# Performance work log

Hardware: AMD Instinct MI355X
Metric: run time of the kernel (lower is better)

The kernel has to match this reference:

```python
import jax, jax.numpy as jnp
import numpy as np

H, N, F = 10, 200000, 128
HID, C = 256, 100
NEG_SLOPE = 0.2

def _leaky(x):
    return jnp.where(x >= 0, x, NEG_SLOPE * x)

def _prelu(x, a):
    return jnp.where(x >= 0, x, a * x)

def setup_inputs() -> dict:
    key = jax.random.key(0)
    ks = jax.random.split(key, 12)
    inp = {
        "features": jax.random.normal(ks[0], (H, N, F), dtype=jnp.float32),
        "label_emb": jax.random.normal(ks[1], (N, C), dtype=jnp.float32),
        # lr_att: Linear(2F, 1) -> weight as [2F] vector + scalar bias
        "W_att": jax.random.normal(ks[2], (2 * F,), dtype=jnp.float32) * 0.05,
        "b_att": jnp.zeros((), dtype=jnp.float32),
        # lr_output = FeedForwardNetII(F, HID, C, n_layers=2): Dense(F,HID), PReLU, Dense(HID,C)
        "Wo1": jax.random.normal(ks[3], (F, HID), dtype=jnp.float32) * 0.05,
        "bo1": jnp.zeros((HID,), dtype=jnp.float32),
        "ao": jnp.asarray(0.25, dtype=jnp.float32),
        "Wo2": jax.random.normal(ks[4], (HID, C), dtype=jnp.float32) * 0.05,
        "bo2": jnp.zeros((C,), dtype=jnp.float32),
        # label_fc = FeedForwardNet(C, HID, C, n_layers=2): Linear(C,HID), PReLU, Linear(HID,C)
        "Wl1": jax.random.normal(ks[5], (C, HID), dtype=jnp.float32) * 0.05,
        "bl1": jnp.zeros((HID,), dtype=jnp.float32),
        "al": jnp.asarray(0.25, dtype=jnp.float32),
        "Wl2": jax.random.normal(ks[6], (HID, C), dtype=jnp.float32) * 0.05,
        "bl2": jnp.zeros((C,), dtype=jnp.float32),
    }
    return inp

def reference(features, label_emb, W_att, b_att, Wo1, bo1, ao, Wo2, bo2,
              Wl1, bl1, al, Wl2, bl2):
    # features: [H, N, F]; dropouts are identity (p=0, eval mode)
    nF = features.shape[-1]
    W1, W2 = W_att[:nF], W_att[nF:]  # cat([history, x_i]) @ W_att == history@W1 + x_i@W2
    x0 = features[0]
    scores = [_leaky(x0 @ (W1 + W2) + b_att)]  # hop 0: cat([x0, x0])
    for i in range(1, features.shape[0]):
        hist_att = jax.nn.softmax(jnp.stack(scores, axis=1), axis=1)  # [N, i]
        history = jnp.einsum('ni,inf->nf', hist_att, features[:i])    # [N, F]
        scores.append(_leaky(history @ W1 + features[i] @ W2 + b_att))
    att = jax.nn.softmax(jnp.stack(scores, axis=1), axis=1)           # [N, H]
    right = jnp.einsum('ni,inf->nf', att, features)                   # [N, F]
    # lr_output: Dense -> PReLU -> Dense
    out = _prelu(right @ Wo1 + bo1, ao) @ Wo2 + bo2                   # [N, C]
    # label branch: label_fc(label_emb)
    out = out + (_prelu(label_emb @ Wl1 + bl1, al) @ Wl2 + bl2)
    return out
```

## Files before the change

kernel.cpp:

```cpp
#include <hip/hip_runtime.h>
#include <cstddef>

#define NHOP 10
#define NN 200000
#define FF 128
#define HIDD 256
#define CCC 100
#define NEG_SLOPE_C 0.2f

typedef __attribute__((ext_vector_type(8))) short bf16x8;
typedef __attribute__((ext_vector_type(4))) short bf16x4;
typedef __attribute__((ext_vector_type(4))) float f32x4;

__device__ __forceinline__ unsigned short f2bf(float x){
  unsigned u = __float_as_uint(x);
  u = u + 0x7FFFu + ((u >> 16) & 1u);
  return (unsigned short)(u >> 16);
}
__device__ __forceinline__ float bf2f(short s){
  return __uint_as_float(((unsigned)(unsigned short)s) << 16);
}

__device__ __forceinline__ f32x4 mfma16(bf16x8 a, bf16x8 b, f32x4 c){
  return __builtin_amdgcn_mfma_f32_16x16x32_bf16(a, b, c, 0, 0, 0);
}

__device__ __forceinline__ float leakyf(float x){ return x >= 0.f ? x : NEG_SLOPE_C*x; }

__global__ __launch_bounds__(256) void prep_weights(
    const float* __restrict__ Wo1, const float* __restrict__ Wl1,
    const float* __restrict__ Wo2, const float* __restrict__ Wl2,
    unsigned short* __restrict__ Wo1T, unsigned short* __restrict__ Wl1T,
    unsigned short* __restrict__ Wo2T, unsigned short* __restrict__ Wl2T)
{
  const int id = blockIdx.x*256 + threadIdx.x;
  {
    const int c = id >> 7, k = id & 127;
    Wo1T[id] = f2bf(Wo1[(size_t)k*HIDD + c]);
    Wl1T[id] = (k < CCC) ? f2bf(Wl1[(size_t)k*HIDD + c]) : 0;
  }
  if (id < 112*256){
    const int c = id >> 8, k = id & 255;
    Wo2T[id] = (c < CCC) ? f2bf(Wo2[(size_t)k*CCC + c]) : 0;
    Wl2T[id] = (c < CCC) ? f2bf(Wl2[(size_t)k*CCC + c]) : 0;
  }
}

__global__ __launch_bounds__(256) void attn_right_kernel(
    const float* __restrict__ feat,
    const float* __restrict__ Watt,
    const float* __restrict__ batt,
    unsigned short* __restrict__ rightb)
{
  const int lane = threadIdx.x & 63;
  const int w = threadIdx.x >> 6;
  const int nl = lane >> 4, fl = lane & 15;
  const int n = blockIdx.x*16 + w*4 + nl;

  const float4 w1a = *reinterpret_cast<const float4*>(Watt + fl*4);
  const float4 w1b = *reinterpret_cast<const float4*>(Watt + 64 + fl*4);
  const float4 w2a = *reinterpret_cast<const float4*>(Watt + FF + fl*4);
  const float4 w2b = *reinterpret_cast<const float4*>(Watt + FF + 64 + fl*4);
  const float b = batt[0];

  float p1[NHOP], p2[NHOP];
  bf16x8 fbf[NHOP];
  const float* fp = feat + (size_t)n*FF;
  #pragma unroll
  for (int i=0;i<NHOP;i++){
    const float* hp = fp + (size_t)i*((size_t)NN*FF);
    const float4 va = *reinterpret_cast<const float4*>(hp + fl*4);
    const float4 vb = *reinterpret_cast<const float4*>(hp + 64 + fl*4);
    p1[i] = va.x*w1a.x + va.y*w1a.y + va.z*w1a.z + va.w*w1a.w
          + vb.x*w1b.x + vb.y*w1b.y + vb.z*w1b.z + vb.w*w1b.w;
    p2[i] = va.x*w2a.x + va.y*w2a.y + va.z*w2a.z + va.w*w2a.w
          + vb.x*w2b.x + vb.y*w2b.y + vb.z*w2b.z + vb.w*w2b.w;
    fbf[i][0]=(short)f2bf(va.x); fbf[i][1]=(short)f2bf(va.y);
    fbf[i][2]=(short)f2bf(va.z); fbf[i][3]=(short)f2bf(va.w);
    fbf[i][4]=(short)f2bf(vb.x); fbf[i][5]=(short)f2bf(vb.y);
    fbf[i][6]=(short)f2bf(vb.z); fbf[i][7]=(short)f2bf(vb.w);
  }
  #pragma unroll
  for (int m=8;m>0;m>>=1){
    #pragma unroll
    for (int i=0;i<NHOP;i++){
      p1[i] += __shfl_xor(p1[i], m, 64);
      p2[i] += __shfl_xor(p2[i], m, 64);
    }
  }
  float sc[NHOP];
  sc[0] = leakyf(p1[0] + p2[0] + b);
  #pragma unroll
  for (int i=1;i<NHOP;i++){
    float mx = sc[0];
    #pragma unroll
    for (int j=1;j<i;j++) mx = fmaxf(mx, sc[j]);
    float Z = 0.f, hs = 0.f;
    #pragma unroll
    for (int j=0;j<i;j++){
      const float e = __expf(sc[j]-mx);
      Z += e;
      hs = fmaf(e, p1[j], hs);
    }
    sc[i] = leakyf(hs/Z + p2[i] + b);
  }
  float mx = sc[0];
  #pragma unroll
  for (int j=1;j<NHOP;j++) mx = fmaxf(mx, sc[j]);
  float Z = 0.f;
  float e[NHOP];
  #pragma unroll
  for (int j=0;j<NHOP;j++){ e[j] = __expf(sc[j]-mx); Z += e[j]; }
  const float inv = 1.f/Z;
  float racc[8];
  #pragma unroll
  for (int u=0;u<8;u++) racc[u] = 0.f;
  #pragma unroll
  for (int j=0;j<NHOP;j++){
    const float a = e[j]*inv;
    #pragma unroll
    for (int u=0;u<8;u++) racc[u] = fmaf(a, bf2f(fbf[j][u]), racc[u]);
  }
  bf16x4 sa, sb;
  sa[0]=(short)f2bf(racc[0]); sa[1]=(short)f2bf(racc[1]);
  sa[2]=(short)f2bf(racc[2]); sa[3]=(short)f2bf(racc[3]);
  sb[0]=(short)f2bf(racc[4]); sb[1]=(short)f2bf(racc[5]);
  sb[2]=(short)f2bf(racc[6]); sb[3]=(short)f2bf(racc[7]);
  *reinterpret_cast<bf16x4*>(rightb + (size_t)n*FF + fl*4) = sa;
  *reinterpret_cast<bf16x4*>(rightb + (size_t)n*FF + 64 + fl*4) = sb;
}

__device__ __forceinline__ void scatter_h(unsigned short* sH, f32x4 h, float bias,
                                          float alpha, int c, int nt, int lq)
{
  #pragma unroll
  for (int j=0;j<4;++j){
    float v = h[j] + bias;
    v = v >= 0.f ? v : alpha*v;
    const int n = nt*16 + lq*4 + j;
    *reinterpret_cast<unsigned short*>((char*)sH + n*512 + ((2*c) ^ ((n&7)<<4))) = f2bf(v);
  }
}

__device__ __forceinline__ void gemm2_accum(const unsigned short* sH,
    const unsigned short* __restrict__ W2T, f32x4 (&o)[2][4],
    const int w, const int lr, const int lq)
{
  #pragma unroll
  for (int i2=0; i2<2; ++i2){
    const int ct2 = 2*w + i2;
    if (ct2 < 7){
      bf16x8 b2[8];
      #pragma unroll
      for (int kk=0; kk<8; ++kk)
        b2[kk] = *reinterpret_cast<const bf16x8*>(W2T + (size_t)(ct2*16+lr)*256 + kk*32 + lq*8);
      #pragma unroll
      for (int nt=0; nt<4; ++nt){
        const int row = nt*16 + lr;
        #pragma unroll
        for (int kk=0; kk<8; ++kk){
          const bf16x8 a2 = *reinterpret_cast<const bf16x8*>(
              (const char*)sH + row*512 + ((kk*64 + lq*16) ^ ((row&7)<<4)));
          o[i2][nt] = mfma16(a2, b2[kk], o[i2][nt]);
        }
      }
    }
  }
}

__device__ __forceinline__ bf16x8 label_frag(const float* __restrict__ label,
                                             size_t gnode, int kk, int lq)
{
  bf16x8 r = (bf16x8){0,0,0,0,0,0,0,0};
  const float* base = label + gnode*CCC;
  if (kk < 3){
    const float4 va = *reinterpret_cast<const float4*>(base + kk*32 + lq*8);
    const float4 vb = *reinterpret_cast<const float4*>(base + kk*32 + lq*8 + 4);
    r[0]=(short)f2bf(va.x); r[1]=(short)f2bf(va.y); r[2]=(short)f2bf(va.z); r[3]=(short)f2bf(va.w);
    r[4]=(short)f2bf(vb.x); r[5]=(short)f2bf(vb.y); r[6]=(short)f2bf(vb.z); r[7]=(short)f2bf(vb.w);
  } else if (lq == 0){
    const float4 va = *reinterpret_cast<const float4*>(base + 96);
    r[0]=(short)f2bf(va.x); r[1]=(short)f2bf(va.y); r[2]=(short)f2bf(va.z); r[3]=(short)f2bf(va.w);
  }
  return r;
}

__global__ __launch_bounds__(256) void mlp_mfma_kernel(
    const unsigned short* __restrict__ rightb, const float* __restrict__ label,
    const unsigned short* __restrict__ Wo1T, const float* __restrict__ bo1, const float* __restrict__ aop,
    const unsigned short* __restrict__ Wo2T, const float* __restrict__ bo2,
    const unsigned short* __restrict__ Wl1T, const float* __restrict__ bl1, const float* __restrict__ alp,
    const unsigned short* __restrict__ Wl2T, const float* __restrict__ bl2,
    float* __restrict__ out)
{
  __shared__ __align__(16) unsigned short sH[64*256];
  const int t = threadIdx.x;
  const int w = t >> 6, lane = t & 63, lr = lane & 15, lq = lane >> 4;
  const size_t nb = (size_t)blockIdx.x * 64;
  const float ao = aop[0], al = alp[0];

  f32x4 o[2][4];
  #pragma unroll
  for (int i2=0; i2<2; ++i2){
    const int ct2 = 2*w + i2;
    const int c2 = ct2*16 + lr;
    const float init = (ct2 < 7 && c2 < CCC) ? (bo2[c2] + bl2[c2]) : 0.f;
    #pragma unroll
    for (int nt=0; nt<4; ++nt) o[i2][nt] = (f32x4){init, init, init, init};
  }

  #pragma unroll
  for (int cc=0; cc<2; ++cc){
    bf16x8 B[2][4];
    float b1c[2];
    #pragma unroll
    for (int ct=0; ct<2; ++ct){
      const int c = (w*4 + cc*2 + ct)*16 + lr;
      b1c[ct] = bo1[c];
      #pragma unroll
      for (int kk=0; kk<4; ++kk)
        B[ct][kk] = *reinterpret_cast<const bf16x8*>(Wo1T + (size_t)c*128 + kk*32 + lq*8);
    }
    #pragma unroll
    for (int nt=0; nt<4; ++nt){
      const int row = nt*16 + lr;
      f32x4 h0 = (f32x4){0.f,0.f,0.f,0.f}, h1 = h0;
      #pragma unroll
      for (int kk=0; kk<4; ++kk){
        const bf16x8 a = *reinterpret_cast<const bf16x8*>(
            rightb + (nb + row)*FF + kk*32 + lq*8);
        h0 = mfma16(a, B[0][kk], h0);
        h1 = mfma16(a, B[1][kk], h1);
      }
      scatter_h(sH, h0, b1c[0], ao, (w*4 + cc*2 + 0)*16 + lr, nt, lq);
      scatter_h(sH, h1, b1c[1], ao, (w*4 + cc*2 + 1)*16 + lr, nt, lq);
    }
  }
  __syncthreads();
  gemm2_accum(sH, Wo2T, o, w, lr, lq);
  __syncthreads();

  #pragma unroll
  for (int cc=0; cc<2; ++cc){
    bf16x8 B[2][4];
    float b1c[2];
    #pragma unroll
    for (int ct=0; ct<2; ++ct){
      const int c = (w*4 + cc*2 + ct)*16 + lr;
      b1c[ct] = bl1[c];
      #pragma unroll
      for (int kk=0; kk<4; ++kk)
        B[ct][kk] = *reinterpret_cast<const bf16x8*>(Wl1T + (size_t)c*128 + kk*32 + lq*8);
    }
    #pragma unroll
    for (int nt=0; nt<4; ++nt){
      const int row = nt*16 + lr;
      f32x4 h0 = (f32x4){0.f,0.f,0.f,0.f}, h1 = h0;
      #pragma unroll
      for (int kk=0; kk<4; ++kk){
        const bf16x8 a = label_frag(label, nb + row, kk, lq);
        h0 = mfma16(a, B[0][kk], h0);
        h1 = mfma16(a, B[1][kk], h1);
      }
      scatter_h(sH, h0, b1c[0], al, (w*4 + cc*2 + 0)*16 + lr, nt, lq);
      scatter_h(sH, h1, b1c[1], al, (w*4 + cc*2 + 1)*16 + lr, nt, lq);
    }
  }
  __syncthreads();
  gemm2_accum(sH, Wl2T, o, w, lr, lq);

  #pragma unroll
  for (int i2=0; i2<2; ++i2){
    const int ct2 = 2*w + i2;
    const int c2 = ct2*16 + lr;
    if (ct2 < 7 && c2 < CCC){
      #pragma unroll
      for (int nt=0; nt<4; ++nt){
        #pragma unroll
        for (int j=0; j<4; ++j){
          const int n = nt*16 + lq*4 + j;
          out[(nb + n)*CCC + c2] = o[i2][nt][j];
        }
      }
    }
  }
}

extern "C" void kernel_launch(void* const* d_in, const int* in_sizes, int n_in,
                              void* d_out, int out_size, void* d_ws, size_t ws_size,
                              hipStream_t stream) {
  const float* feat  = (const float*)d_in[0];
  const float* label = (const float*)d_in[1];
  const float* Watt  = (const float*)d_in[2];
  const float* batt  = (const float*)d_in[3];
  const float* Wo1   = (const float*)d_in[4];
  const float* bo1   = (const float*)d_in[5];
  const float* aop   = (const float*)d_in[6];
  const float* Wo2   = (const float*)d_in[7];
  const float* bo2   = (const float*)d_in[8];
  const float* Wl1   = (const float*)d_in[9];
  const float* bl1   = (const float*)d_in[10];
  const float* alp   = (const float*)d_in[11];
  const float* Wl2   = (const float*)d_in[12];
  const float* bl2   = (const float*)d_in[13];
  float* out = (float*)d_out;

  unsigned short* rightb = (unsigned short*)d_ws;
  unsigned short* Wo1T = rightb + (size_t)NN*FF;
  unsigned short* Wl1T = Wo1T + 256*128;
  unsigned short* Wo2T = Wl1T + 256*128;
  unsigned short* Wl2T = Wo2T + 112*256;

  prep_weights<<<128, 256, 0, stream>>>(Wo1, Wl1, Wo2, Wl2, Wo1T, Wl1T, Wo2T, Wl2T);
  attn_right_kernel<<<NN/16, 256, 0, stream>>>(feat, Watt, batt, rightb);
  mlp_mfma_kernel<<<NN/64, 256, 0, stream>>>(rightb, label,
                                             Wo1T, bo1, aop, Wo2T, bo2,
                                             Wl1T, bl1, alp, Wl2T, bl2, out);
}
```

Measured before the change: 400.3 us.

## Fuse attention and MLP kernels, stage activations and label through shared memory

```diff
diff --git a/kernel.cpp b/kernel.cpp
--- a/kernel.cpp
+++ b/kernel.cpp
@@ -1,4 +1,5 @@
 #include <hip/hip_runtime.h>
+#include <hip/hip_bf16.h>
 #include <cstddef>
 
 #define NHOP 10
@@ -12,19 +13,15 @@
 typedef __attribute__((ext_vector_type(4))) short bf16x4;
 typedef __attribute__((ext_vector_type(4))) float f32x4;
 
-__device__ __forceinline__ unsigned short f2bf(float x){
-  unsigned u = __float_as_uint(x);
-  u = u + 0x7FFFu + ((u >> 16) & 1u);
-  return (unsigned short)(u >> 16);
+__device__ __forceinline__ short f2bfs(float x){
+  return __builtin_bit_cast(short, __float2bfloat16(x));
 }
 __device__ __forceinline__ float bf2f(short s){
   return __uint_as_float(((unsigned)(unsigned short)s) << 16);
 }
-
 __device__ __forceinline__ f32x4 mfma16(bf16x8 a, bf16x8 b, f32x4 c){
   return __builtin_amdgcn_mfma_f32_16x16x32_bf16(a, b, c, 0, 0, 0);
 }
-
 __device__ __forceinline__ float leakyf(float x){ return x >= 0.f ? x : NEG_SLOPE_C*x; }
 
 __global__ __launch_bounds__(256) void prep_weights(
@@ -36,98 +33,14 @@
   const int id = blockIdx.x*256 + threadIdx.x;
   {
     const int c = id >> 7, k = id & 127;
-    Wo1T[id] = f2bf(Wo1[(size_t)k*HIDD + c]);
-    Wl1T[id] = (k < CCC) ? f2bf(Wl1[(size_t)k*HIDD + c]) : 0;
+    Wo1T[id] = (unsigned short)f2bfs(Wo1[(size_t)k*HIDD + c]);
+    Wl1T[id] = (k < CCC) ? (unsigned short)f2bfs(Wl1[(size_t)k*HIDD + c]) : 0;
   }
   if (id < 112*256){
     const int c = id >> 8, k = id & 255;
-    Wo2T[id] = (c < CCC) ? f2bf(Wo2[(size_t)k*CCC + c]) : 0;
-    Wl2T[id] = (c < CCC) ? f2bf(Wl2[(size_t)k*CCC + c]) : 0;
-  }
-}
-
-__global__ __launch_bounds__(256) void attn_right_kernel(
-    const float* __restrict__ feat,
-    const float* __restrict__ Watt,
-    const float* __restrict__ batt,
-    unsigned short* __restrict__ rightb)
-{
-  const int lane = threadIdx.x & 63;
-  const int w = threadIdx.x >> 6;
-  const int nl = lane >> 4, fl = lane & 15;
-  const int n = blockIdx.x*16 + w*4 + nl;
-
-  const float4 w1a = *reinterpret_cast<const float4*>(Watt + fl*4);
-  const float4 w1b = *reinterpret_cast<const float4*>(Watt + 64 + fl*4);
-  const float4 w2a = *reinterpret_cast<const float4*>(Watt + FF + fl*4);
-  const float4 w2b = *reinterpret_cast<const float4*>(Watt + FF + 64 + fl*4);
-  const float b = batt[0];
-
-  float p1[NHOP], p2[NHOP];
-  bf16x8 fbf[NHOP];
-  const float* fp = feat + (size_t)n*FF;
-  #pragma unroll
-  for (int i=0;i<NHOP;i++){
-    const float* hp = fp + (size_t)i*((size_t)NN*FF);
-    const float4 va = *reinterpret_cast<const float4*>(hp + fl*4);
-    const float4 vb = *reinterpret_cast<const float4*>(hp + 64 + fl*4);
-    p1[i] = va.x*w1a.x + va.y*w1a.y + va.z*w1a.z + va.w*w1a.w
-          + vb.x*w1b.x + vb.y*w1b.y + vb.z*w1b.z + vb.w*w1b.w;
-    p2[i] = va.x*w2a.x + va.y*w2a.y + va.z*w2a.z + va.w*w2a.w
-          + vb.x*w2b.x + vb.y*w2b.y + vb.z*w2b.z + vb.w*w2b.w;
-    fbf[i][0]=(short)f2bf(va.x); fbf[i][1]=(short)f2bf(va.y);
-    fbf[i][2]=(short)f2bf(va.z); fbf[i][3]=(short)f2bf(va.w);
-    fbf[i][4]=(short)f2bf(vb.x); fbf[i][5]=(short)f2bf(vb.y);
-    fbf[i][6]=(short)f2bf(vb.z); fbf[i][7]=(short)f2bf(vb.w);
-  }
-  #pragma unroll
-  for (int m=8;m>0;m>>=1){
-    #pragma unroll
-    for (int i=0;i<NHOP;i++){
-      p1[i] += __shfl_xor(p1[i], m, 64);
-      p2[i] += __shfl_xor(p2[i], m, 64);
-    }
-  }
-  float sc[NHOP];
-  sc[0] = leakyf(p1[0] + p2[0] + b);
-  #pragma unroll
-  for (int i=1;i<NHOP;i++){
-    float mx = sc[0];
-    #pragma unroll
-    for (int j=1;j<i;j++) mx = fmaxf(mx, sc[j]);
-    float Z = 0.f, hs = 0.f;
-    #pragma unroll
-    for (int j=0;j<i;j++){
-      const float e = __expf(sc[j]-mx);
-      Z += e;
-      hs = fmaf(e, p1[j], hs);
-    }
-    sc[i] = leakyf(hs/Z + p2[i] + b);
-  }
-  float mx = sc[0];
-  #pragma unroll
-  for (int j=1;j<NHOP;j++) mx = fmaxf(mx, sc[j]);
-  float Z = 0.f;
-  float e[NHOP];
-  #pragma unroll
-  for (int j=0;j<NHOP;j++){ e[j] = __expf(sc[j]-mx); Z += e[j]; }
-  const float inv = 1.f/Z;
-  float racc[8];
-  #pragma unroll
-  for (int u=0;u<8;u++) racc[u] = 0.f;
-  #pragma unroll
-  for (int j=0;j<NHOP;j++){
-    const float a = e[j]*inv;
-    #pragma unroll
-    for (int u=0;u<8;u++) racc[u] = fmaf(a, bf2f(fbf[j][u]), racc[u]);
-  }
-  bf16x4 sa, sb;
-  sa[0]=(short)f2bf(racc[0]); sa[1]=(short)f2bf(racc[1]);
-  sa[2]=(short)f2bf(racc[2]); sa[3]=(short)f2bf(racc[3]);
-  sb[0]=(short)f2bf(racc[4]); sb[1]=(short)f2bf(racc[5]);
-  sb[2]=(short)f2bf(racc[6]); sb[3]=(short)f2bf(racc[7]);
-  *reinterpret_cast<bf16x4*>(rightb + (size_t)n*FF + fl*4) = sa;
-  *reinterpret_cast<bf16x4*>(rightb + (size_t)n*FF + 64 + fl*4) = sb;
+    Wo2T[id] = (c < CCC) ? (unsigned short)f2bfs(Wo2[(size_t)k*CCC + c]) : 0;
+    Wl2T[id] = (c < CCC) ? (unsigned short)f2bfs(Wl2[(size_t)k*CCC + c]) : 0;
+  }
 }
 
 __device__ __forceinline__ void scatter_h(unsigned short* sH, f32x4 h, float bias,
@@ -138,7 +51,41 @@
     float v = h[j] + bias;
     v = v >= 0.f ? v : alpha*v;
     const int n = nt*16 + lq*4 + j;
-    *reinterpret_cast<unsigned short*>((char*)sH + n*512 + ((2*c) ^ ((n&7)<<4))) = f2bf(v);
+    *reinterpret_cast<unsigned short*>((char*)sH + n*512 + ((2*c) ^ ((n&7)<<4))) =
+        (unsigned short)f2bfs(v);
+  }
+}
+
+__device__ __forceinline__ void gemm1(const unsigned short* sA, unsigned short* sH,
+    const unsigned short* __restrict__ W1T, const float* __restrict__ b1, const float alpha,
+    const int w, const int lr, const int lq)
+{
+  #pragma unroll
+  for (int cc=0; cc<2; ++cc){
+    bf16x8 B[2][4];
+    float b1c[2];
+    #pragma unroll
+    for (int ct=0; ct<2; ++ct){
+      const int c = (w*4 + cc*2 + ct)*16 + lr;
+      b1c[ct] = b1[c];
+      #pragma unroll
+      for (int kk=0; kk<4; ++kk)
+        B[ct][kk] = *reinterpret_cast<const bf16x8*>(W1T + (size_t)c*128 + kk*32 + lq*8);
+    }
+    #pragma unroll
+    for (int nt=0; nt<4; ++nt){
+      const int row = nt*16 + lr;
+      f32x4 h0 = (f32x4){0.f,0.f,0.f,0.f}, h1 = h0;
+      #pragma unroll
+      for (int kk=0; kk<4; ++kk){
+        const bf16x8 a = *reinterpret_cast<const bf16x8*>(
+            (const char*)sA + row*256 + ((kk*64 + lq*16) ^ ((row&7)<<4)));
+        h0 = mfma16(a, B[0][kk], h0);
+        h1 = mfma16(a, B[1][kk], h1);
+      }
+      scatter_h(sH, h0, b1c[0], alpha, (w*4 + cc*2 + 0)*16 + lr, nt, lq);
+      scatter_h(sH, h1, b1c[1], alpha, (w*4 + cc*2 + 1)*16 + lr, nt, lq);
+    }
   }
 }
 
@@ -168,36 +115,95 @@
   }
 }
 
-__device__ __forceinline__ bf16x8 label_frag(const float* __restrict__ label,
-                                             size_t gnode, int kk, int lq)
-{
-  bf16x8 r = (bf16x8){0,0,0,0,0,0,0,0};
-  const float* base = label + gnode*CCC;
-  if (kk < 3){
-    const float4 va = *reinterpret_cast<const float4*>(base + kk*32 + lq*8);
-    const float4 vb = *reinterpret_cast<const float4*>(base + kk*32 + lq*8 + 4);
-    r[0]=(short)f2bf(va.x); r[1]=(short)f2bf(va.y); r[2]=(short)f2bf(va.z); r[3]=(short)f2bf(va.w);
-    r[4]=(short)f2bf(vb.x); r[5]=(short)f2bf(vb.y); r[6]=(short)f2bf(vb.z); r[7]=(short)f2bf(vb.w);
-  } else if (lq == 0){
-    const float4 va = *reinterpret_cast<const float4*>(base + 96);
-    r[0]=(short)f2bf(va.x); r[1]=(short)f2bf(va.y); r[2]=(short)f2bf(va.z); r[3]=(short)f2bf(va.w);
-  }
-  return r;
-}
-
-__global__ __launch_bounds__(256) void mlp_mfma_kernel(
-    const unsigned short* __restrict__ rightb, const float* __restrict__ label,
+__global__ __launch_bounds__(256) void gamlp_fused(
+    const float* __restrict__ feat, const float* __restrict__ label,
+    const float* __restrict__ Watt, const float* __restrict__ batt,
     const unsigned short* __restrict__ Wo1T, const float* __restrict__ bo1, const float* __restrict__ aop,
     const unsigned short* __restrict__ Wo2T, const float* __restrict__ bo2,
     const unsigned short* __restrict__ Wl1T, const float* __restrict__ bl1, const float* __restrict__ alp,
     const unsigned short* __restrict__ Wl2T, const float* __restrict__ bl2,
     float* __restrict__ out)
 {
+  __shared__ __align__(16) unsigned short sA[64*128];
   __shared__ __align__(16) unsigned short sH[64*256];
   const int t = threadIdx.x;
   const int w = t >> 6, lane = t & 63, lr = lane & 15, lq = lane >> 4;
+  const int nl = lq, fl = lr;
   const size_t nb = (size_t)blockIdx.x * 64;
   const float ao = aop[0], al = alp[0];
+
+  const float4 w1a = *reinterpret_cast<const float4*>(Watt + fl*4);
+  const float4 w1b = *reinterpret_cast<const float4*>(Watt + 64 + fl*4);
+  const float4 w2a = *reinterpret_cast<const float4*>(Watt + FF + fl*4);
+  const float4 w2b = *reinterpret_cast<const float4*>(Watt + FF + 64 + fl*4);
+  const float batt0 = batt[0];
+
+  #pragma unroll 1
+  for (int it=0; it<4; ++it){
+    const int row = w*16 + it*4 + nl;
+    const float* fp = feat + (nb + row)*FF;
+    float p1[NHOP], p2[NHOP];
+    bf16x8 fbf[NHOP];
+    #pragma unroll
+    for (int i=0;i<NHOP;i++){
+      const float* hp = fp + (size_t)i*((size_t)NN*FF);
+      const float4 va = *reinterpret_cast<const float4*>(hp + fl*4);
+      const float4 vb = *reinterpret_cast<const float4*>(hp + 64 + fl*4);
+      p1[i] = va.x*w1a.x + va.y*w1a.y + va.z*w1a.z + va.w*w1a.w
+            + vb.x*w1b.x + vb.y*w1b.y + vb.z*w1b.z + vb.w*w1b.w;
+      p2[i] = va.x*w2a.x + va.y*w2a.y + va.z*w2a.z + va.w*w2a.w
+            + vb.x*w2b.x + vb.y*w2b.y + vb.z*w2b.z + vb.w*w2b.w;
+      fbf[i][0]=f2bfs(va.x); fbf[i][1]=f2bfs(va.y); fbf[i][2]=f2bfs(va.z); fbf[i][3]=f2bfs(va.w);
+      fbf[i][4]=f2bfs(vb.x); fbf[i][5]=f2bfs(vb.y); fbf[i][6]=f2bfs(vb.z); fbf[i][7]=f2bfs(vb.w);
+    }
+    #pragma unroll
+    for (int m=8;m>0;m>>=1){
+      #pragma unroll
+      for (int i=0;i<NHOP;i++){
+        p1[i] += __shfl_xor(p1[i], m, 64);
+        p2[i] += __shfl_xor(p2[i], m, 64);
+      }
+    }
+    float sc[NHOP];
+    sc[0] = leakyf(p1[0] + p2[0] + batt0);
+    #pragma unroll
+    for (int i=1;i<NHOP;i++){
+      float mx = sc[0];
+      #pragma unroll
+      for (int j=1;j<i;j++) mx = fmaxf(mx, sc[j]);
+      float Z = 0.f, hs = 0.f;
+      #pragma unroll
+      for (int j=0;j<i;j++){
+        const float e = __expf(sc[j]-mx);
+        Z += e;
+        hs = fmaf(e, p1[j], hs);
+      }
+      sc[i] = leakyf(hs/Z + p2[i] + batt0);
+    }
+    float mx = sc[0];
+    #pragma unroll
+    for (int j=1;j<NHOP;j++) mx = fmaxf(mx, sc[j]);
+    float Z = 0.f;
+    float e[NHOP];
+    #pragma unroll
+    for (int j=0;j<NHOP;j++){ e[j] = __expf(sc[j]-mx); Z += e[j]; }
+    const float inv = 1.f/Z;
+    float racc[8];
+    #pragma unroll
+    for (int u=0;u<8;u++) racc[u] = 0.f;
+    #pragma unroll
+    for (int j=0;j<NHOP;j++){
+      const float a = e[j]*inv;
+      #pragma unroll
+      for (int u=0;u<8;u++) racc[u] = fmaf(a, bf2f(fbf[j][u]), racc[u]);
+    }
+    bf16x4 sa, sb;
+    sa[0]=f2bfs(racc[0]); sa[1]=f2bfs(racc[1]); sa[2]=f2bfs(racc[2]); sa[3]=f2bfs(racc[3]);
+    sb[0]=f2bfs(racc[4]); sb[1]=f2bfs(racc[5]); sb[2]=f2bfs(racc[6]); sb[3]=f2bfs(racc[7]);
+    *reinterpret_cast<bf16x4*>((char*)sA + row*256 + ((fl*8) ^ ((row&7)<<4))) = sa;
+    *reinterpret_cast<bf16x4*>((char*)sA + row*256 + ((128 + fl*8) ^ ((row&7)<<4))) = sb;
+  }
+  __syncthreads();
 
   f32x4 o[2][4];
   #pragma unroll
@@ -209,66 +215,32 @@
     for (int nt=0; nt<4; ++nt) o[i2][nt] = (f32x4){init, init, init, init};
   }
 
-  #pragma unroll
-  for (int cc=0; cc<2; ++cc){
-    bf16x8 B[2][4];
-    float b1c[2];
-    #pragma unroll
-    for (int ct=0; ct<2; ++ct){
-      const int c = (w*4 + cc*2 + ct)*16 + lr;
-      b1c[ct] = bo1[c];
-      #pragma unroll
-      for (int kk=0; kk<4; ++kk)
-        B[ct][kk] = *reinterpret_cast<const bf16x8*>(Wo1T + (size_t)c*128 + kk*32 + lq*8);
-    }
-    #pragma unroll
-    for (int nt=0; nt<4; ++nt){
-      const int row = nt*16 + lr;
-      f32x4 h0 = (f32x4){0.f,0.f,0.f,0.f}, h1 = h0;
-      #pragma unroll
-      for (int kk=0; kk<4; ++kk){
-        const bf16x8 a = *reinterpret_cast<const bf16x8*>(
-            rightb + (nb + row)*FF + kk*32 + lq*8);
-        h0 = mfma16(a, B[0][kk], h0);
-        h1 = mfma16(a, B[1][kk], h1);
-      }
-      scatter_h(sH, h0, b1c[0], ao, (w*4 + cc*2 + 0)*16 + lr, nt, lq);
-      scatter_h(sH, h1, b1c[1], ao, (w*4 + cc*2 + 1)*16 + lr, nt, lq);
-    }
-  }
-  __syncthreads();
+  gemm1(sA, sH, Wo1T, bo1, ao, w, lr, lq);
+  __syncthreads();
+
+  {
+    const int rw = t >> 2, q = t & 3;
+    const float* lbase = label + (nb + rw)*CCC;
+    #pragma unroll
+    for (int u=0; u<8; ++u){
+      const int c0 = q*32 + u*4;
+      bf16x4 pv = (bf16x4){0,0,0,0};
+      if (c0 < CCC){
+        const float4 v = *reinterpret_cast<const float4*>(lbase + c0);
+        pv[0]=f2bfs(v.x); pv[1]=f2bfs(v.y); pv[2]=f2bfs(v.z); pv[3]=f2bfs(v.w);
+      }
+      *reinterpret_cast<bf16x4*>((char*)sA + rw*256 + ((2*c0) ^ ((rw&7)<<4))) = pv;
+    }
+  }
   gemm2_accum(sH, Wo2T, o, w, lr, lq);
   __syncthreads();
 
-  #pragma unroll
-  for (int cc=0; cc<2; ++cc){
-    bf16x8 B[2][4];
-    float b1c[2];
-    #pragma unroll
-    for (int ct=0; ct<2; ++ct){
-      const int c = (w*4 + cc*2 + ct)*16 + lr;
-      b1c[ct] = bl1[c];
-      #pragma unroll
-      for (int kk=0; kk<4; ++kk)
-        B[ct][kk] = *reinterpret_cast<const bf16x8*>(Wl1T + (size_t)c*128 + kk*32 + lq*8);
-    }
-    #pragma unroll
-    for (int nt=0; nt<4; ++nt){
-      const int row = nt*16 + lr;
-      f32x4 h0 = (f32x4){0.f,0.f,0.f,0.f}, h1 = h0;
-      #pragma unroll
-      for (int kk=0; kk<4; ++kk){
-        const bf16x8 a = label_frag(label, nb + row, kk, lq);
-        h0 = mfma16(a, B[0][kk], h0);
-        h1 = mfma16(a, B[1][kk], h1);
-      }
-      scatter_h(sH, h0, b1c[0], al, (w*4 + cc*2 + 0)*16 + lr, nt, lq);
-      scatter_h(sH, h1, b1c[1], al, (w*4 + cc*2 + 1)*16 + lr, nt, lq);
-    }
-  }
+  gemm1(sA, sH, Wl1T, bl1, al, w, lr, lq);
   __syncthreads();
   gemm2_accum(sH, Wl2T, o, w, lr, lq);
-
+  __syncthreads();
+
+  float* sF = reinterpret_cast<float*>(sH);
   #pragma unroll
   for (int i2=0; i2<2; ++i2){
     const int ct2 = 2*w + i2;
@@ -277,12 +249,16 @@
       #pragma unroll
       for (int nt=0; nt<4; ++nt){
         #pragma unroll
-        for (int j=0; j<4; ++j){
-          const int n = nt*16 + lq*4 + j;
-          out[(nb + n)*CCC + c2] = o[i2][nt][j];
-        }
-      }
-    }
+        for (int j=0; j<4; ++j)
+          sF[(nt*16 + lq*4 + j)*CCC + c2] = o[i2][nt][j];
+      }
+    }
+  }
+  __syncthreads();
+  #pragma unroll
+  for (int p=0; p<25; ++p){
+    const int idx = p*256 + t;
+    out[nb*CCC + idx] = sF[idx];
   }
 }
 
@@ -305,15 +281,13 @@
   const float* bl2   = (const float*)d_in[13];
   float* out = (float*)d_out;
 
-  unsigned short* rightb = (unsigned short*)d_ws;
-  unsigned short* Wo1T = rightb + (size_t)NN*FF;
+  unsigned short* Wo1T = (unsigned short*)d_ws;
   unsigned short* Wl1T = Wo1T + 256*128;
   unsigned short* Wo2T = Wl1T + 256*128;
   unsigned short* Wl2T = Wo2T + 112*256;
 
   prep_weights<<<128, 256, 0, stream>>>(Wo1, Wl1, Wo2, Wl2, Wo1T, Wl1T, Wo2T, Wl2T);
-  attn_right_kernel<<<NN/16, 256, 0, stream>>>(feat, Watt, batt, rightb);
-  mlp_mfma_kernel<<<NN/64, 256, 0, stream>>>(rightb, label,
-                                             Wo1T, bo1, aop, Wo2T, bo2,
-                                             Wl1T, bl1, alp, Wl2T, bl2, out);
-}
+  gamlp_fused<<<NN/64, 256, 0, stream>>>(feat, label, Watt, batt,
+                                         Wo1T, bo1, aop, Wo2T, bo2,
+                                         Wl1T, bl1, alp, Wl2T, bl2, out);
+}
```

New measurement: 423.1 us. 5.7% more time.

## Map one wavefront per node in attention kernel and use library bf16 conversion

Applied to the files above, without the earlier changes.

```diff
diff --git a/kernel.cpp b/kernel.cpp
--- a/kernel.cpp
+++ b/kernel.cpp
@@ -1,4 +1,5 @@
 #include <hip/hip_runtime.h>
+#include <hip/hip_bf16.h>
 #include <cstddef>
 
 #define NHOP 10
@@ -12,19 +13,12 @@
 typedef __attribute__((ext_vector_type(4))) short bf16x4;
 typedef __attribute__((ext_vector_type(4))) float f32x4;
 
-__device__ __forceinline__ unsigned short f2bf(float x){
-  unsigned u = __float_as_uint(x);
-  u = u + 0x7FFFu + ((u >> 16) & 1u);
-  return (unsigned short)(u >> 16);
-}
-__device__ __forceinline__ float bf2f(short s){
-  return __uint_as_float(((unsigned)(unsigned short)s) << 16);
-}
-
+__device__ __forceinline__ short f2bfs(float x){
+  return __builtin_bit_cast(short, __float2bfloat16(x));
+}
 __device__ __forceinline__ f32x4 mfma16(bf16x8 a, bf16x8 b, f32x4 c){
   return __builtin_amdgcn_mfma_f32_16x16x32_bf16(a, b, c, 0, 0, 0);
 }
-
 __device__ __forceinline__ float leakyf(float x){ return x >= 0.f ? x : NEG_SLOPE_C*x; }
 
 __global__ __launch_bounds__(256) void prep_weights(
@@ -36,13 +30,13 @@
   const int id = blockIdx.x*256 + threadIdx.x;
   {
     const int c = id >> 7, k = id & 127;
-    Wo1T[id] = f2bf(Wo1[(size_t)k*HIDD + c]);
-    Wl1T[id] = (k < CCC) ? f2bf(Wl1[(size_t)k*HIDD + c]) : 0;
+    Wo1T[id] = (unsigned short)f2bfs(Wo1[(size_t)k*HIDD + c]);
+    Wl1T[id] = (k < CCC) ? (unsigned short)f2bfs(Wl1[(size_t)k*HIDD + c]) : 0;
   }
   if (id < 112*256){
     const int c = id >> 8, k = id & 255;
-    Wo2T[id] = (c < CCC) ? f2bf(Wo2[(size_t)k*CCC + c]) : 0;
-    Wl2T[id] = (c < CCC) ? f2bf(Wl2[(size_t)k*CCC + c]) : 0;
+    Wo2T[id] = (c < CCC) ? (unsigned short)f2bfs(Wo2[(size_t)k*CCC + c]) : 0;
+    Wl2T[id] = (c < CCC) ? (unsigned short)f2bfs(Wl2[(size_t)k*CCC + c]) : 0;
   }
 }
 
@@ -53,35 +47,23 @@
     unsigned short* __restrict__ rightb)
 {
   const int lane = threadIdx.x & 63;
-  const int w = threadIdx.x >> 6;
-  const int nl = lane >> 4, fl = lane & 15;
-  const int n = blockIdx.x*16 + w*4 + nl;
-
-  const float4 w1a = *reinterpret_cast<const float4*>(Watt + fl*4);
-  const float4 w1b = *reinterpret_cast<const float4*>(Watt + 64 + fl*4);
-  const float4 w2a = *reinterpret_cast<const float4*>(Watt + FF + fl*4);
-  const float4 w2b = *reinterpret_cast<const float4*>(Watt + FF + 64 + fl*4);
+  const int n = blockIdx.x * 4 + (threadIdx.x >> 6);
+
+  const float2 w1 = *reinterpret_cast<const float2*>(Watt + 2*lane);
+  const float2 w2 = *reinterpret_cast<const float2*>(Watt + FF + 2*lane);
   const float b = batt[0];
 
+  float2 f[NHOP];
   float p1[NHOP], p2[NHOP];
-  bf16x8 fbf[NHOP];
-  const float* fp = feat + (size_t)n*FF;
+  const float* fp = feat + (size_t)n*FF + 2*lane;
   #pragma unroll
   for (int i=0;i<NHOP;i++){
-    const float* hp = fp + (size_t)i*((size_t)NN*FF);
-    const float4 va = *reinterpret_cast<const float4*>(hp + fl*4);
-    const float4 vb = *reinterpret_cast<const float4*>(hp + 64 + fl*4);
-    p1[i] = va.x*w1a.x + va.y*w1a.y + va.z*w1a.z + va.w*w1a.w
-          + vb.x*w1b.x + vb.y*w1b.y + vb.z*w1b.z + vb.w*w1b.w;
-    p2[i] = va.x*w2a.x + va.y*w2a.y + va.z*w2a.z + va.w*w2a.w
-          + vb.x*w2b.x + vb.y*w2b.y + vb.z*w2b.z + vb.w*w2b.w;
-    fbf[i][0]=(short)f2bf(va.x); fbf[i][1]=(short)f2bf(va.y);
-    fbf[i][2]=(short)f2bf(va.z); fbf[i][3]=(short)f2bf(va.w);
-    fbf[i][4]=(short)f2bf(vb.x); fbf[i][5]=(short)f2bf(vb.y);
-    fbf[i][6]=(short)f2bf(vb.z); fbf[i][7]=(short)f2bf(vb.w);
-  }
-  #pragma unroll
-  for (int m=8;m>0;m>>=1){
+    f[i] = *reinterpret_cast<const float2*>(fp + (size_t)i*((size_t)NN*FF));
+    p1[i] = f[i].x*w1.x + f[i].y*w1.y;
+    p2[i] = f[i].x*w2.x + f[i].y*w2.y;
+  }
+  #pragma unroll
+  for (int m=32;m>0;m>>=1){
     #pragma unroll
     for (int i=0;i<NHOP;i++){
       p1[i] += __shfl_xor(p1[i], m, 64);
@@ -112,22 +94,15 @@
   #pragma unroll
   for (int j=0;j<NHOP;j++){ e[j] = __expf(sc[j]-mx); Z += e[j]; }
   const float inv = 1.f/Z;
-  float racc[8];
-  #pragma unroll
-  for (int u=0;u<8;u++) racc[u] = 0.f;
+  float rx = 0.f, ry = 0.f;
   #pragma unroll
   for (int j=0;j<NHOP;j++){
     const float a = e[j]*inv;
-    #pragma unroll
-    for (int u=0;u<8;u++) racc[u] = fmaf(a, bf2f(fbf[j][u]), racc[u]);
-  }
-  bf16x4 sa, sb;
-  sa[0]=(short)f2bf(racc[0]); sa[1]=(short)f2bf(racc[1]);
-  sa[2]=(short)f2bf(racc[2]); sa[3]=(short)f2bf(racc[3]);
-  sb[0]=(short)f2bf(racc[4]); sb[1]=(short)f2bf(racc[5]);
-  sb[2]=(short)f2bf(racc[6]); sb[3]=(short)f2bf(racc[7]);
-  *reinterpret_cast<bf16x4*>(rightb + (size_t)n*FF + fl*4) = sa;
-  *reinterpret_cast<bf16x4*>(rightb + (size_t)n*FF + 64 + fl*4) = sb;
+    rx = fmaf(a, f[j].x, rx);
+    ry = fmaf(a, f[j].y, ry);
+  }
+  ushort2 st; st.x = (unsigned short)f2bfs(rx); st.y = (unsigned short)f2bfs(ry);
+  *reinterpret_cast<ushort2*>(rightb + (size_t)n*FF + 2*lane) = st;
 }
 
 __device__ __forceinline__ void scatter_h(unsigned short* sH, f32x4 h, float bias,
@@ -138,7 +113,8 @@
     float v = h[j] + bias;
     v = v >= 0.f ? v : alpha*v;
     const int n = nt*16 + lq*4 + j;
-    *reinterpret_cast<unsigned short*>((char*)sH + n*512 + ((2*c) ^ ((n&7)<<4))) = f2bf(v);
+    *reinterpret_cast<unsigned short*>((char*)sH + n*512 + ((2*c) ^ ((n&7)<<4))) =
+        (unsigned short)f2bfs(v);
   }
 }
 
@@ -176,11 +152,11 @@
   if (kk < 3){
     const float4 va = *reinterpret_cast<const float4*>(base + kk*32 + lq*8);
     const float4 vb = *reinterpret_cast<const float4*>(base + kk*32 + lq*8 + 4);
-    r[0]=(short)f2bf(va.x); r[1]=(short)f2bf(va.y); r[2]=(short)f2bf(va.z); r[3]=(short)f2bf(va.w);
-    r[4]=(short)f2bf(vb.x); r[5]=(short)f2bf(vb.y); r[6]=(short)f2bf(vb.z); r[7]=(short)f2bf(vb.w);
+    r[0]=f2bfs(va.x); r[1]=f2bfs(va.y); r[2]=f2bfs(va.z); r[3]=f2bfs(va.w);
+    r[4]=f2bfs(vb.x); r[5]=f2bfs(vb.y); r[6]=f2bfs(vb.z); r[7]=f2bfs(vb.w);
   } else if (lq == 0){
     const float4 va = *reinterpret_cast<const float4*>(base + 96);
-    r[0]=(short)f2bf(va.x); r[1]=(short)f2bf(va.y); r[2]=(short)f2bf(va.z); r[3]=(short)f2bf(va.w);
+    r[0]=f2bfs(va.x); r[1]=f2bfs(va.y); r[2]=f2bfs(va.z); r[3]=f2bfs(va.w);
   }
   return r;
 }
@@ -312,7 +288,7 @@
   unsigned short* Wl2T = Wo2T + 112*256;
 
   prep_weights<<<128, 256, 0, stream>>>(Wo1, Wl1, Wo2, Wl2, Wo1T, Wl1T, Wo2T, Wl2T);
-  attn_right_kernel<<<NN/16, 256, 0, stream>>>(feat, Watt, batt, rightb);
+  attn_right_kernel<<<NN/4, 256, 0, stream>>>(feat, Watt, batt, rightb);
   mlp_mfma_kernel<<<NN/64, 256, 0, stream>>>(rightb, label,
                                              Wo1T, bo1, aop, Wo2T, bo2,
                                              Wl1T, bl1, alp, Wl2T, bl2, out);
```

After: 462.4 us. 1.16x slower.
